# Performance work log

Hardware: AMD Instinct MI355X
Metric: run time of the kernel (lower is better)

Reference implementation:

```python
import math
import jax, jax.numpy as jnp
import numpy as np

K = 8
C = 16
MODES = 64
LEVELS = 0
CK = C * K


def _legendre_filters(k):
    """Numpy port of get_filter('legendre', k). Returns ec_s, ec_d, rc_e, rc_o (float32)."""
    from numpy.polynomial import Polynomial
    phi_c = np.zeros((k, k))
    phi2_c = np.zeros((k, k))
    for ki in range(k):
        P = np.polynomial.legendre.Legendre.basis(ki).convert(kind=Polynomial)
        c1 = P(Polynomial([-1.0, 2.0])).coef
        phi_c[ki, :len(c1)] = np.sqrt(2 * ki + 1) * c1
        c2 = P(Polynomial([-1.0, 4.0])).coef
        phi2_c[ki, :len(c2)] = np.sqrt(2.0) * np.sqrt(2 * ki + 1) * c2
    psi1 = phi2_c.copy()
    psi2 = phi2_c.copy()

    def proj_half(a, b):  # integral over [0,0.5] of poly product
        prod = np.convolve(a, b)
        prod[np.abs(prod) < 1e-10] = 0.0
        i = np.arange(len(prod))
        return np.sum(prod / (i + 1) * 0.5 ** (i + 1))

    for ki in range(k):
        a = phi2_c[ki, :ki + 1]
        for i in range(k):
            p = proj_half(a, phi_c[i, :i + 1])
            psi1[ki] -= p * phi_c[i]
            psi2[ki] -= p * phi_c[i]
        for j in range(ki):
            p = proj_half(a, psi1[j])
            psi1[ki] -= p * psi1[j]
            psi2[ki] -= p * psi2[j]
        prod1 = np.convolve(psi1[ki], psi1[ki])
        i1 = np.arange(len(prod1))
        norm1 = np.sum(prod1 / (i1 + 1) * 0.5 ** (i1 + 1))
        prod2 = np.convolve(psi2[ki], psi2[ki])
        i2 = np.arange(len(prod2))
        norm2 = np.sum(prod2 / (i2 + 1) * (1 - 0.5 ** (i2 + 1)))
        nrm = math.sqrt(max(norm1 + norm2, 1e-16))
        psi1[ki] /= nrm
        psi2[ki] /= nrm

    xg, wg = np.polynomial.legendre.leggauss(k)
    x_m = (xg + 1.0) / 2.0
    wm = wg / 2.0
    pv = lambda c, t: np.polynomial.polynomial.polyval(t, c)
    H0 = np.zeros((k, k)); H1 = np.zeros((k, k))
    G0 = np.zeros((k, k)); G1 = np.zeros((k, k))
    s2 = 1.0 / math.sqrt(2.0)
    for ki in range(k):
        for kp in range(k):
            pk = pv(phi_c[kp], x_m)
            H0[ki, kp] = s2 * np.sum(wm * pv(phi_c[ki], x_m / 2) * pk)
            G0[ki, kp] = s2 * np.sum(wm * pv(psi1[ki], x_m / 2) * pk)        # t<=0.5 -> psi1
            H1[ki, kp] = s2 * np.sum(wm * pv(phi_c[ki], (x_m + 1) / 2) * pk)
            G1[ki, kp] = s2 * np.sum(wm * pv(psi2[ki], (x_m + 1) / 2) * pk)  # t>0.5 -> psi2
    for m in (H0, H1, G0, G1):
        m[np.abs(m) < 1e-10] = 0.0
    # PHI0 = PHI1 = I, so H0r = H0 etc.
    ec_s = np.concatenate([H0.T, H1.T], axis=0).astype(np.float32)  # [2k,k]
    ec_d = np.concatenate([G0.T, G1.T], axis=0).astype(np.float32)
    rc_e = np.concatenate([H0, G0], axis=0).astype(np.float32)
    rc_o = np.concatenate([H1, G1], axis=0).astype(np.float32)
    return ec_s, ec_d, rc_e, rc_o


def setup_inputs() -> dict:
    key = jax.random.key(0)
    ks = jax.random.split(key, 7)
    B, N = 16, 8192
    x = jax.random.normal(ks[0], (B, N, C, K), dtype=jnp.float32)
    scale = 1.0 / (CK ** 0.5 + 1e-6)
    mk = lambda kk: scale * jax.random.normal(kk, (CK, CK, MODES), dtype=jnp.float32)
    ec_s, ec_d, rc_e, rc_o = _legendre_filters(K)
    return {
        "x": x,
        "A_wr": mk(ks[1]), "A_wi": mk(ks[2]),
        "B_wr": mk(ks[3]), "B_wi": mk(ks[4]),
        "C_wr": mk(ks[5]), "C_wi": mk(ks[6]),
        "ln_w": jnp.ones((CK,), jnp.float32),
        "ln_b": jnp.zeros((CK,), jnp.float32),
        "ec_s": jnp.asarray(ec_s), "ec_d": jnp.asarray(ec_d),
        "rc_e": jnp.asarray(rc_e), "rc_o": jnp.asarray(rc_o),
    }


def _spectral(v, wr, wi):
    # SparseKernelFT1d: rfft over N (ortho), truncate to `modes`, complex mix, irfft.
    b, n, c, k = v.shape
    vf = v.reshape(b, n, c * k)
    ft = jnp.fft.rfft(vf, axis=1, norm="ortho")           # [b, n//2+1, ck] complex
    l = min(MODES, ft.shape[1])
    w = wr[:, :, :l] + 1j * wi[:, :, :l]                   # [ck, ck, l]
    out = jnp.einsum("bxi,iox->bxo", ft[:, :l], w)
    out = jnp.pad(out, ((0, 0), (0, ft.shape[1] - l), (0, 0)))
    o = jnp.fft.irfft(out, n=n, axis=1, norm="ortho")
    return o.reshape(b, n, c, k)


def reference(x, A_wr, A_wi, B_wr, B_wi, C_wr, C_wi, ln_w, ln_b, ec_s, ec_d, rc_e, rc_o):
    B_, N0, c, k = x.shape
    nl = 2 ** math.ceil(math.log2(max(N0, 1)))
    if nl > N0:
        x = jnp.pad(x, ((0, 0), (0, nl - N0), (0, 0), (0, 0)))
    ns = int(math.log2(nl))
    Ud, Us = [], []
    for _ in range(ns - LEVELS):
        # one-level wavelet decomposition: even/odd gather + small [2k,k] matmuls
        xa = jnp.concatenate([x[:, ::2], x[:, 1::2]], axis=-1)  # [B, n/2, c, 2k]
        d = xa @ ec_d
        x = xa @ ec_s
        Ud.append(_spectral(d, A_wr, A_wi) + _spectral(x, B_wr, B_wi))
        Us.append(_spectral(d, C_wr, C_wi))
    # LayerNorm over flattened c*k, then exact GELU (torch default)
    b, n, cc, kk = x.shape
    xf = x.reshape(b, n, cc * kk)
    mu = jnp.mean(xf, axis=-1, keepdims=True)
    var = jnp.var(xf, axis=-1, keepdims=True)
    xf = (xf - mu) / jnp.sqrt(var + 1e-5) * ln_w + ln_b
    x = jax.nn.gelu(xf.reshape(b, n, cc, kk), approximate=False)
    for i in range(ns - 1 - LEVELS, -1, -1):
        x = x + Us[i]
        xc = jnp.concatenate([x, Ud[i]], axis=-1)              # [B, n, c, 2k]
        x_e = xc @ rc_e
        x_o = xc @ rc_o
        # interleave even/odd along N
        x = jnp.stack([x_e, x_o], axis=2).reshape(b, x_e.shape[1] * 2, cc, kk)
    return x[:, :N0]
```

## Files before the change

### kernel.cpp

```cpp
#include <hip/hip_runtime.h>
#include <math.h>

typedef unsigned short bfu;
typedef short bf16x8 __attribute__((ext_vector_type(8)));
typedef float f32x4 __attribute__((ext_vector_type(4)));

__device__ __forceinline__ float bs2f(bfu s){
  union{ unsigned int u; float f; } v; v.u = ((unsigned int)s) << 16; return v.f;
}
__device__ __forceinline__ bfu f2bs(float f){
  union{ float ff; unsigned int u; } v; v.ff = f;
  unsigned int u = v.u;
  unsigned int r = (u + 0x7fffu + ((u >> 16) & 1u)) >> 16;
  return (bfu)r;
}

struct LevelTab { int twoff[13]; int ll[13]; int logh[13]; };
struct WPtrs { const void* p[6]; };
struct FwTab { int pcum[7]; int h[6]; int np[6]; int twF[6]; long lvl[6]; long ftp[6]; };
struct DpTab { long lvl[7]; long ftp[7]; long yt[7]; int twD[7]; int h[7]; int l[7]; int lgh[7]; };
struct PrTab { int np[13]; int l[13]; long ftp[13]; long xa[13]; };
struct MxTab { int fcum[13]; int h[13]; long xa[13]; long yt[13]; };
struct IvTab { int bxcum[6]; int h[6]; int twF[6]; long yt[6]; long lvl[6]; };

__global__ __launch_bounds__(256) void k_sniff(const bfu* __restrict__ x, int* __restrict__ flag){
  __shared__ int cnt;
  if(threadIdx.x==0) cnt = 0;
  __syncthreads();
  int c = 0;
  for(int j=threadIdx.x; j<4096; j+=256){
    bfu v = x[2*j];
    int e = (v>>7)&0xFF;
    if(e >= 0xC0) c++;
  }
  atomicAdd(&cnt, c);
  __syncthreads();
  if(threadIdx.x==0) flag[0] = (cnt > 64) ? 1 : 0;
}

__global__ __launch_bounds__(256) void k_cvt_small(
    const void* lnw, const void* lnb, const void* ecs, const void* ecd,
    const void* rce, const void* rco, bfu* __restrict__ CSM, const int* __restrict__ FLAG){
  int f32 = FLAG[0];
  const void* src[6] = {ecs, ecd, rce, rco, lnw, lnb};
  int tid = threadIdx.x;
  for(int a=0; a<6; ++a)
    for(int j=tid; j<128; j+=256)
      CSM[a*128+j] = f32 ? f2bs(((const float*)src[a])[j]) : ((const bfu*)src[a])[j];
}

__global__ __launch_bounds__(256) void k_wtrans(WPtrs wp, bfu* __restrict__ W2, const int* __restrict__ FLAG){
  int f32 = FLAG[0];
  int o = blockIdx.x;
  int w = blockIdx.y;
  __shared__ bfu tile[64][130];
  int tid = threadIdx.x;
  const void* src = wp.p[w];
  if(f32){
    const float* s = (const float*)src;
    #pragma unroll
    for(int it=0; it<8; ++it){
      int e = it*256 + tid;
      int i = e >> 4, fq = e & 15;
      float4 v = *reinterpret_cast<const float4*>(s + ((size_t)i*128 + o)*64 + fq*4);
      tile[fq*4+0][i] = f2bs(v.x);
      tile[fq*4+1][i] = f2bs(v.y);
      tile[fq*4+2][i] = f2bs(v.z);
      tile[fq*4+3][i] = f2bs(v.w);
    }
  } else {
    const bfu* s = (const bfu*)src;
    #pragma unroll
    for(int it=0; it<4; ++it){
      int e = it*256 + tid;
      int i = e >> 3, fq = e & 7;
      union{uint4 u; bfu x[8];} U;
      U.u = *reinterpret_cast<const uint4*>(s + ((size_t)i*128 + o)*64 + fq*8);
      #pragma unroll
      for(int j=0;j<8;++j) tile[fq*8+j][i] = U.x[j];
    }
  }
  __syncthreads();
  bfu* dst = W2 + (size_t)w*64*128*128 + (size_t)o*128;
  #pragma unroll
  for(int it=0; it<8; ++it){
    int e = it*256 + tid;
    int f = e >> 5, iq = e & 31;
    union{uint2 u; bfu x[4];} P;
    #pragma unroll
    for(int j=0;j<4;++j) P.x[j] = tile[f][iq*4+j];
    *reinterpret_cast<uint2*>(dst + (size_t)f*128*128 + iq*4) = P.u;
  }
}

__global__ __launch_bounds__(256) void k_twgenF(bfu* __restrict__ TWF, bfu* __restrict__ TWI){
  int e = blockIdx.x*256 + threadIdx.x;
  int kind = blockIdx.y;
  const int offs[7] = {0,524288,786432,917504,983040,1015808,1032192};
  int le = 5;
  #pragma unroll
  for(int i=0;i<6;++i){ if(e < offs[i+1]){ le = i; break; } }
  int rem = e - offs[le];
  int logh = 12 - le;
  int h = 1 << logh;
  int f, t, neg;
  if(kind==0){ int r = rem >> logh; t = rem & (h-1); f = (r<64)?r:(r-64); neg = (r>=64); }
  else       { t = rem >> 7; int f2 = rem & 127;     f = (f2<64)?f2:(f2-64); neg = (f2>=64); }
  int m = (f*t) & (h-1);
  float th = 6.283185307179586f * ((float)m / (float)h);
  float s, c; sincosf(th, &s, &c);
  float val = neg ? -s : c;
  if(kind==0) TWF[e] = f2bs(val); else TWI[e] = f2bs(val);
}

__global__ __launch_bounds__(256) void k_twgen(LevelTab lt, float* __restrict__ tw){
  int lev = blockIdx.y;
  int logh = lt.logh[lev];
  int h = 1 << logh;
  int l = lt.ll[lev];
  int tot = l*h;
  int idx = blockIdx.x*256 + threadIdx.x;
  if(idx >= tot) return;
  int t = idx & (h-1);
  int f = idx >> logh;
  int m = (f*t) & (h-1);
  float th = 6.283185307179586f * ((float)m / (float)h);
  float s, c; sincosf(th, &s, &c);
  tw[lt.twoff[lev] + idx] = c;
  tw[lt.twoff[lev] + tot + idx] = s;
}

__global__ __launch_bounds__(256) void k_decomp0(
    const void* __restrict__ xin, bfu* __restrict__ dT, bfu* __restrict__ sT,
    const bfu* __restrict__ CSM, int h, const int* __restrict__ FLAG)
{
  int f32 = FLAG[0];
  __shared__ float ls[64][132];
  __shared__ bfu sdo[128][36];
  __shared__ bfu sso[128][36];
  __shared__ float Fd[16][8], Fs[16][8];
  int tid = threadIdx.x;
  if(tid < 128){ Fs[tid>>3][tid&7] = bs2f(CSM[tid]); Fd[tid>>3][tid&7] = bs2f(CSM[128+tid]); }
  int b = blockIdx.y;
  int t0in = blockIdx.x * 64;
  if(f32){
    const float* src = (const float*)xin + ((size_t)b*2*h + t0in)*128;
    #pragma unroll
    for(int it=0; it<8; ++it){
      int e = it*256 + tid;
      int row = e>>5, cq = e&31;
      float4 v = *reinterpret_cast<const float4*>(src + (size_t)row*128 + cq*4);
      ls[row][cq*4+0]=v.x; ls[row][cq*4+1]=v.y; ls[row][cq*4+2]=v.z; ls[row][cq*4+3]=v.w;
    }
  } else {
    const bfu* src = (const bfu*)xin + ((size_t)b*2*h + t0in)*128;
    #pragma unroll
    for(int it=0; it<4; ++it){
      int e = it*256 + tid;
      int row = e>>4, cq = e&15;
      union{uint4 u; bfu x[8];} U;
      U.u = *reinterpret_cast<const uint4*>(src + (size_t)row*128 + cq*8);
      #pragma unroll
      for(int j=0;j<8;++j) ls[row][cq*8+j] = bs2f(U.x[j]);
    }
  }
  __syncthreads();
  int g = tid>>7, ch = tid&127;
  int c = ch>>3, kp = ch&7;
  float fdE[8], fdO[8], fsE[8], fsO[8];
  #pragma unroll
  for(int j=0;j<8;++j){ fdE[j]=Fd[j][kp]; fdO[j]=Fd[8+j][kp]; fsE[j]=Fs[j][kp]; fsO[j]=Fs[8+j][kp]; }
  union{ uint2 u; bfu x[4]; } Dq, Sq;
  #pragma unroll
  for(int tl=0; tl<16; ++tl){
    int rl = 2*(g*16+tl);
    const float* ev = &ls[rl][c*8];
    const float* od = &ls[rl+1][c*8];
    float d=0.f, s=0.f;
    #pragma unroll
    for(int j=0;j<8;++j){
      d += ev[j]*fdE[j] + od[j]*fdO[j];
      s += ev[j]*fsE[j] + od[j]*fsO[j];
    }
    Dq.x[tl&3] = f2bs(d); Sq.x[tl&3] = f2bs(s);
    if((tl&3)==3){
      int tb = g*16 + (tl & ~3);
      *reinterpret_cast<uint2*>(&sdo[ch][tb]) = Dq.u;
      *reinterpret_cast<uint2*>(&sso[ch][tb]) = Sq.u;
    }
  }
  __syncthreads();
  size_t obase = (size_t)b*128*h + (t0in>>1);
  #pragma unroll
  for(int it=0; it<4; ++it){
    int e = it*256 + tid;
    int r = e >> 3, kq = e & 7;
    union{uint2 u; bfu x[4];} P;
    #pragma unroll
    for(int j=0;j<4;++j) P.x[j] = sdo[r][kq*4+j];
    *reinterpret_cast<uint2*>(dT + obase + (size_t)r*h + kq*4) = P.u;
  }
  #pragma unroll
  for(int it=0; it<4; ++it){
    int e = it*256 + tid;
    int r = e >> 3, kq = e & 7;
    union{uint2 u; bfu x[4];} P;
    #pragma unroll
    for(int j=0;j<4;++j) P.x[j] = sso[r][kq*4+j];
    *reinterpret_cast<uint2*>(sT + obase + (size_t)r*h + kq*4) = P.u;
  }
}

__global__ __launch_bounds__(256) void k_decompT_big(
    const bfu* __restrict__ inT, bfu* __restrict__ dT, bfu* __restrict__ sT,
    const bfu* __restrict__ CSM, int h)
{
  __shared__ float Fd[16][8], Fs[16][8];
  int tid = threadIdx.x;
  if(tid < 128){ Fs[tid>>3][tid&7] = bs2f(CSM[tid]); Fd[tid>>3][tid&7] = bs2f(CSM[128+tid]); }
  __syncthreads();
  int tt0 = blockIdx.x * 256;
  int b = blockIdx.y, c = blockIdx.z;
  int kp = tid >> 5, tq = tid & 31;
  float fdE[8], fdO[8], fsE[8], fsO[8];
  #pragma unroll
  for(int k=0;k<8;++k){ fdE[k]=Fd[k][kp]; fdO[k]=Fd[8+k][kp]; fsE[k]=Fs[k][kp]; fsO[k]=Fs[8+k][kp]; }
  const bfu* base = inT + ((size_t)b*128 + c*8)*(size_t)(2*h) + (size_t)2*tt0 + tq*16;
  union{uint4 u[2]; bfu x[16];} E[8];
  #pragma unroll
  for(int k=0;k<8;++k){
    E[k].u[0] = *reinterpret_cast<const uint4*>(base + (size_t)k*(2*h));
    E[k].u[1] = *reinterpret_cast<const uint4*>(base + (size_t)k*(2*h) + 8);
  }
  union{uint4 u; bfu x[8];} Od, Os;
  #pragma unroll
  for(int to=0; to<8; ++to){
    float d=0.f, s=0.f;
    #pragma unroll
    for(int k=0;k<8;++k){
      float ev = bs2f(E[k].x[2*to]), od = bs2f(E[k].x[2*to+1]);
      d += ev*fdE[k] + od*fdO[k];
      s += ev*fsE[k] + od*fsO[k];
    }
    Od.x[to] = f2bs(d); Os.x[to] = f2bs(s);
  }
  size_t ob = ((size_t)b*128 + c*8 + kp)*h + tt0 + tq*8;
  *reinterpret_cast<uint4*>(dT + ob) = Od.u;
  *reinterpret_cast<uint4*>(sT + ob) = Os.u;
}

__global__ __launch_bounds__(256) void k_decompT(
    const bfu* __restrict__ inT, bfu* __restrict__ dT, bfu* __restrict__ sT,
    const bfu* __restrict__ CSM, int h, int total)
{
  __shared__ float Fd[16][8], Fs[16][8];
  int tid = threadIdx.x;
  if(tid < 128){ Fs[tid>>3][tid&7] = bs2f(CSM[tid]); Fd[tid>>3][tid&7] = bs2f(CSM[128+tid]); }
  __syncthreads();
  int idx = blockIdx.x*256 + tid;
  if(idx >= total) return;
  if(h >= 4){
    int nto = h>>2;
    int to = idx & (nto-1);
    int bc = idx / nto;
    int c = bc & 15, b = bc >> 4;
    const bfu* base = inT + ((size_t)b*128 + c*8)*(size_t)(2*h) + to*8;
    float d8[4][8] = {}, s8[4][8] = {};
    #pragma unroll
    for(int k=0;k<8;++k){
      union{uint4 u; bfu x[8];} U;
      U.u = *reinterpret_cast<const uint4*>(base + (size_t)k*(2*h));
      const float* fdE = Fd[k]; const float* fdO = Fd[8+k];
      const float* fsE = Fs[k]; const float* fsO = Fs[8+k];
      #pragma unroll
      for(int tl=0; tl<4; ++tl){
        float ev = bs2f(U.x[2*tl]), od = bs2f(U.x[2*tl+1]);
        #pragma unroll
        for(int kp=0;kp<8;++kp){
          d8[tl][kp] += ev*fdE[kp] + od*fdO[kp];
          s8[tl][kp] += ev*fsE[kp] + od*fsO[kp];
        }
      }
    }
    #pragma unroll
    for(int kp=0;kp<8;++kp){
      union{uint2 u; bfu x[4];} Od, Os;
      #pragma unroll
      for(int tl=0;tl<4;++tl){ Od.x[tl]=f2bs(d8[tl][kp]); Os.x[tl]=f2bs(s8[tl][kp]); }
      size_t ob = ((size_t)b*128 + c*8 + kp)*h + to*4;
      *reinterpret_cast<uint2*>(dT + ob) = Od.u;
      *reinterpret_cast<uint2*>(sT + ob) = Os.u;
    }
  } else {
    int c = idx & 15, b = idx >> 4;
    const bfu* base = inT + ((size_t)b*128 + c*8)*(size_t)(2*h);
    for(int tl=0; tl<h; ++tl){
      float d8[8]={}, s8[8]={};
      for(int k=0;k<8;++k){
        float ev = bs2f(base[(size_t)k*2*h + 2*tl]);
        float od = bs2f(base[(size_t)k*2*h + 2*tl+1]);
        #pragma unroll
        for(int kp=0;kp<8;++kp){
          d8[kp] += ev*Fd[k][kp] + od*Fd[8+k][kp];
          s8[kp] += ev*Fs[k][kp] + od*Fs[8+k][kp];
        }
      }
      for(int kp=0;kp<8;++kp){
        size_t ob = ((size_t)b*128 + c*8 + kp)*h + tl;
        dT[ob] = f2bs(d8[kp]); sT[ob] = f2bs(s8[kp]);
      }
    }
  }
}

__global__ __launch_bounds__(256) void k_fwdft_all(
    const bfu* __restrict__ DTall, const bfu* __restrict__ STall,
    const bfu* __restrict__ TWF, float* __restrict__ FTPa, FwTab ft)
{
  int gp = blockIdx.x, b = blockIdx.y;
  int sig = blockIdx.z >> 1, rh = blockIdx.z & 1;
  int lev = 0;
  for(int i=5;i>0;--i){ if(gp >= ft.pcum[i]){ lev = i; break; } }
  int p = gp - ft.pcum[lev];
  int h = ft.h[lev];
  int Kpart = h / ft.np[lev];
  const bfu* SIG = (sig ? STall : DTall) + ft.lvl[lev] + (size_t)b*128*h;
  const bfu* TWr = TWF + ft.twF[lev] + (size_t)(rh*64)*h;
  __shared__ bfu lsA[64*72];
  __shared__ bfu lsB[128*72];
  int tid = threadIdx.x;
  int wave = tid>>6, lane = tid&63;
  int mh = (wave>>1)*32, nh = (wave&1)*64;
  int ml = lane&15, q = lane>>4;
  f32x4 acc[2][4];
  #pragma unroll
  for(int i=0;i<2;++i){
    #pragma unroll
    for(int j=0;j<4;++j) acc[i][j] = (f32x4)0.f;
  }
  int k0base = p*Kpart;
  for(int kc=0; kc<Kpart; kc+=64){
    int k0 = k0base + kc;
    #pragma unroll
    for(int it=0; it<2; ++it){
      int slot = it*256 + tid;
      int row = slot>>3, kq = slot&7;
      *reinterpret_cast<uint4*>(&lsA[row*72 + kq*8]) =
        *reinterpret_cast<const uint4*>(&TWr[(size_t)row*h + k0 + kq*8]);
    }
    #pragma unroll
    for(int it=0; it<4; ++it){
      int slot = it*256 + tid;
      int row = slot>>3, kq = slot&7;
      *reinterpret_cast<uint4*>(&lsB[row*72 + kq*8]) =
        *reinterpret_cast<const uint4*>(&SIG[(size_t)row*h + k0 + kq*8]);
    }
    __syncthreads();
    #pragma unroll
    for(int kk=0; kk<64; kk+=32){
      bf16x8 af[2], bfr[4];
      #pragma unroll
      for(int mi=0;mi<2;++mi)
        af[mi] = *reinterpret_cast<const bf16x8*>(&lsA[(mh+mi*16+ml)*72 + kk + q*8]);
      #pragma unroll
      for(int ni=0;ni<4;++ni)
        bfr[ni] = *reinterpret_cast<const bf16x8*>(&lsB[(nh+ni*16+ml)*72 + kk + q*8]);
      #pragma unroll
      for(int mi=0;mi<2;++mi){
        #pragma unroll
        for(int ni=0;ni<4;++ni)
          acc[mi][ni] = __builtin_amdgcn_mfma_f32_16x16x32_bf16(af[mi], bfr[ni], acc[mi][ni], 0,0,0);
      }
    }
    __syncthreads();
  }
  float* dst = FTPa + ft.ftp[lev] + (((size_t)p*2 + sig)*16 + b)*16384;
  #pragma unroll
  for(int mi=0;mi<2;++mi){
    #pragma unroll
    for(int ni=0;ni<4;++ni){
      int row = rh*64 + mh + mi*16 + q*4;
      int col = nh + ni*16 + ml;
      #pragma unroll
      for(int r=0;r<4;++r)
        dst[(size_t)(row+r)*128 + col] = acc[mi][ni][r];
    }
  }
}

__global__ __launch_bounds__(256) void k_fwdeep_all(
    const bfu* __restrict__ DTall, const bfu* __restrict__ STall,
    float* __restrict__ FTPa, const float* __restrict__ TWD, DpTab dp)
{
  int b = blockIdx.x, sig = blockIdx.y, j = blockIdx.z;
  int h = dp.h[j], l = dp.l[j], logh = dp.lgh[j];
  const bfu* src = (sig? STall : DTall) + dp.lvl[j] + (size_t)b*128*h;
  float* dst = FTPa + dp.ftp[j] + ((size_t)sig*16 + b)*16384;
  const float* TWc = TWD + dp.twD[j];
  __shared__ float s_sig[128*65];
  __shared__ float s_twc[33*64];
  __shared__ float s_tws[33*64];
  int tid = threadIdx.x;
  int hp = h + 1;
  for(int e = tid; e < 128*h; e += 256){
    int ch = e >> logh, t = e & (h-1);
    s_sig[ch*hp + t] = bs2f(src[e]);
  }
  int lh = l*h;
  const float* TWs = TWc + (size_t)lh;
  for(int e = tid; e < lh; e += 256){ s_twc[e] = TWc[e]; s_tws[e] = TWs[e]; }
  __syncthreads();
  for(int idx = tid; idx < l*128; idx += 256){
    int f = idx >> 7, ch = idx & 127;
    const float* sp = &s_sig[ch*hp];
    const float* cp = &s_twc[f*h];
    const float* zp = &s_tws[f*h];
    float re = 0.f, im = 0.f;
    for(int t=0; t<h; ++t){ float v = sp[t]; re += v*cp[t]; im -= v*zp[t]; }
    dst[(size_t)f*128 + ch] = re;
    dst[(size_t)(64+f)*128 + ch] = im;
  }
}

__global__ __launch_bounds__(256) void k_ftpred_all(
    const float* __restrict__ FTPa, bfu* __restrict__ XAa, PrTab pt)
{
  int lev = blockIdx.y;
  int e = blockIdx.x*256 + threadIdx.x;
  const size_t PS = (size_t)2*16*128*128;
  int ch4 = e & 31;
  int row = (e>>5) & 127;
  int b   = (e>>12) & 15;
  int sig = e>>16;
  int f = row & 63, im = row >> 6;
  if(f >= pt.l[lev]) return;
  const float* F = FTPa + pt.ftp[lev];
  int np = pt.np[lev];
  size_t src = (((size_t)sig*16 + b)*128 + row)*128 + (size_t)ch4*4;
  f32x4 v = *reinterpret_cast<const f32x4*>(&F[src]);
  for(int p=1;p<np;++p)
    v += *reinterpret_cast<const f32x4*>(&F[src + (size_t)p*PS]);
  int ch = ch4*4;
  union{ uint2 u; bfu x[4]; } P1, P3;
  #pragma unroll
  for(int j=0;j<4;++j){
    float vj = v[j];
    P1.x[j] = f2bs(im ? -vj : vj);
    P3.x[j] = f2bs(vj);
  }
  bfu* XA = XAa + pt.xa[lev];
  size_t base = (size_t)f*32*512;
  *reinterpret_cast<uint2*>(&XA[base + (size_t)b*512 + sig*256 + im*128 + ch]) = P1.u;
  *reinterpret_cast<uint2*>(&XA[base + (size_t)(16+b)*512 + sig*256 + (1-im)*128 + ch]) = P3.u;
}

__global__ __launch_bounds__(256) void k_modemix_all(
    const bfu* __restrict__ XAa, const bfu* __restrict__ W2,
    bfu* __restrict__ YTa, MxTab mt)
{
  int x = blockIdx.x;
  int lev = 0;
  for(int i=12;i>0;--i){ if(x >= mt.fcum[i]){ lev = i; break; } }
  int f = x - mt.fcum[lev];
  int h = mt.h[lev];
  int obase = blockIdx.y * 16;
  int tid = threadIdx.x;
  int wid = tid>>6, lane = tid&63;
  int m = wid & 1, part = wid >> 1;
  int ml = lane & 15, q = lane >> 4;
  const size_t WSZ = (size_t)64*128*128;
  const bfu* Ab = XAa + mt.xa[lev] + ((size_t)f*32 + m*16 + ml)*512 + q*8;
  const bfu* Wb = W2 + ((size_t)f*128 + obase + ml)*128 + q*8;
  f32x4 acc = (f32x4)0.f;
  if(part == 0){
    #pragma unroll
    for(int ks=0; ks<16; ++ks){
      bf16x8 A = *reinterpret_cast<const bf16x8*>(Ab + ks*32);
      bf16x8 B = *reinterpret_cast<const bf16x8*>(Wb + (size_t)(ks>>2)*WSZ + (ks&3)*32);
      acc = __builtin_amdgcn_mfma_f32_16x16x32_bf16(A, B, acc, 0,0,0);
    }
  } else {
    #pragma unroll
    for(int ks=0; ks<8; ++ks){
      bf16x8 A = *reinterpret_cast<const bf16x8*>(Ab + ks*32);
      bf16x8 B = *reinterpret_cast<const bf16x8*>(Wb + (size_t)(4 + (ks>>2))*WSZ + (ks&3)*32);
      acc = __builtin_amdgcn_mfma_f32_16x16x32_bf16(A, B, acc, 0,0,0);
    }
  }
  bool edge = (f==0) || (2*f == h);
  float sc = edge ? 1.0f/(float)h : 2.0f/(float)h;
  int fo = m ? (64+f) : f;
  int o = obase + ml;
  bfu* dst = YTa + mt.yt[lev] + (part ? (size_t)16*128*128 : 0);
  #pragma unroll
  for(int r=0;r<4;++r){
    int b = q*4 + r;
    float val = acc[r]*sc;
    if(m && edge) val = 0.f;
    dst[((size_t)b*128 + o)*128 + fo] = f2bs(val);
  }
}

__global__ __launch_bounds__(256) void k_invdft_all(
    const bfu* __restrict__ YTa, const bfu* __restrict__ TWI,
    bfu* __restrict__ UdAll, bfu* __restrict__ UsAll, IvTab iv)
{
  int x = blockIdx.x, b = blockIdx.y, u = blockIdx.z;
  int lev = 0;
  for(int i=5;i>0;--i){ if(x >= iv.bxcum[i]){ lev = i; break; } }
  int bx = x - iv.bxcum[lev];
  int h = iv.h[lev];
  bfu* outp = (u ? UsAll : UdAll) + iv.lvl[lev];
  const bfu* Y = YTa + iv.yt[lev] + ((size_t)u*16 + b)*16384;
  const bfu* TWIl = TWI + iv.twF[lev];
  int t0 = bx*128;
  __shared__ bfu lsA[128*136];
  __shared__ bfu lsB[128*136];
  int tid = threadIdx.x;
  #pragma unroll
  for(int it=0; it<8; ++it){
    int slot = it*256 + tid;
    int row = slot>>4, kq = slot&15;
    *reinterpret_cast<uint4*>(&lsA[row*136 + kq*8]) =
      *reinterpret_cast<const uint4*>(&TWIl[(size_t)(t0+row)*128 + kq*8]);
    *reinterpret_cast<uint4*>(&lsB[row*136 + kq*8]) =
      *reinterpret_cast<const uint4*>(&Y[(size_t)row*128 + kq*8]);
  }
  __syncthreads();
  int wave = tid>>6, lane = tid&63;
  int mh = (wave>>1)*64, nh = (wave&1)*64;
  int ml = lane&15, q = lane>>4;
  f32x4 acc[4][4];
  #pragma unroll
  for(int i=0;i<4;++i){
    #pragma unroll
    for(int j=0;j<4;++j) acc[i][j] = (f32x4)0.f;
  }
  #pragma unroll
  for(int kk=0; kk<128; kk+=32){
    bf16x8 af[4], bfr[4];
    #pragma unroll
    for(int mi=0;mi<4;++mi)
      af[mi] = *reinterpret_cast<const bf16x8*>(&lsA[(mh+mi*16+ml)*136 + kk + q*8]);
    #pragma unroll
    for(int ni=0;ni<4;++ni)
      bfr[ni] = *reinterpret_cast<const bf16x8*>(&lsB[(nh+ni*16+ml)*136 + kk + q*8]);
    #pragma unroll
    for(int mi=0;mi<4;++mi){
      #pragma unroll
      for(int ni=0;ni<4;++ni)
        acc[mi][ni] = __builtin_amdgcn_mfma_f32_16x16x32_bf16(af[mi], bfr[ni], acc[mi][ni], 0,0,0);
    }
  }
  #pragma unroll
  for(int mi=0;mi<4;++mi){
    #pragma unroll
    for(int ni=0;ni<4;++ni){
      int row = mh + mi*16 + q*4;
      int col = nh + ni*16 + ml;
      #pragma unroll
      for(int r=0;r<4;++r)
        outp[((size_t)b*h + t0+row+r)*128 + col] = f2bs(acc[mi][ni][r]);
    }
  }
}

__global__ __launch_bounds__(256) void k_invdeep_all(
    const bfu* __restrict__ YTa, bfu* __restrict__ UdAll, bfu* __restrict__ UsAll,
    const float* __restrict__ TWD, DpTab dp)
{
  int b = blockIdx.x, u = blockIdx.y, j = blockIdx.z;
  int h = dp.h[j], l = dp.l[j];
  bfu* outp = (u? UsAll : UdAll) + dp.lvl[j] + (size_t)b*h*128;
  const bfu* Y = YTa + dp.yt[j] + ((size_t)u*16 + b)*16384;
  const float* TWc = TWD + dp.twD[j];
  __shared__ float s_yr[128*66];
  __shared__ float s_yi[128*66];
  __shared__ float s_twc[33*64];
  __shared__ float s_tws[33*64];
  int tid = threadIdx.x;
  #pragma unroll
  for(int it=0; it<8; ++it){
    int slot = it*256 + tid;
    int ch = slot >> 4, kq = slot & 15;
    union{uint4 u4; bfu x[8];} U;
    U.u4 = *reinterpret_cast<const uint4*>(&Y[(size_t)ch*128 + kq*8]);
    if(kq < 8){
      #pragma unroll
      for(int jj=0;jj<8;++jj) s_yr[ch*66 + kq*8 + jj] = bs2f(U.x[jj]);
    } else {
      #pragma unroll
      for(int jj=0;jj<8;++jj) s_yi[ch*66 + (kq-8)*8 + jj] = bs2f(U.x[jj]);
    }
  }
  int lh = l*h;
  const float* TWs = TWc + (size_t)lh;
  for(int e = tid; e < lh; e += 256){ s_twc[e] = TWc[e]; s_tws[e] = TWs[e]; }
  __syncthreads();
  for(int idx = tid; idx < h*128; idx += 256){
    int t = idx >> 7, ch = idx & 127;
    const float* yr = &s_yr[ch*66];
    const float* yi = &s_yi[ch*66];
    float a = 0.f;
    for(int f=0; f<l; ++f)
      a += yr[f]*s_twc[f*h + t] - yi[f]*s_tws[f*h + t];
    outp[idx] = f2bs(a);
  }
}

__global__ __launch_bounds__(128) void k_lngelu(
    const bfu* __restrict__ xin, const bfu* __restrict__ CSM, bfu* __restrict__ xout)
{
  int b = blockIdx.x, tid = threadIdx.x;
  float v = bs2f(xin[b*128 + tid]);
  float s1 = v, s2 = v*v;
  #pragma unroll
  for(int o=32; o; o>>=1){ s1 += __shfl_down(s1,o); s2 += __shfl_down(s2,o); }
  __shared__ float red[2][2];
  int w = tid >> 6;
  if((tid & 63) == 0){ red[w][0]=s1; red[w][1]=s2; }
  __syncthreads();
  float m  = (red[0][0]+red[1][0]) * (1.0f/128.0f);
  float ms = (red[0][1]+red[1][1]) * (1.0f/128.0f);
  float var = ms - m*m;
  float xn = (v - m) * rsqrtf(var + 1e-5f) * bs2f(CSM[512+tid]) + bs2f(CSM[640+tid]);
  float g = 0.5f * xn * (1.0f + erff(xn * 0.70710678118654752f));
  xout[b*128 + tid] = f2bs(g);
}

__global__ __launch_bounds__(256) void k_recon(
    const bfu* __restrict__ xin, const bfu* __restrict__ usp, const bfu* __restrict__ udp,
    const bfu* __restrict__ CSM, void* __restrict__ xout, int h, int logh,
    int is_final, const int* __restrict__ FLAG)
{
  int f32 = is_final ? FLAG[0] : 0;
  __shared__ float Fe[16][8], Fo[16][8];
  int tid = threadIdx.x;
  if(tid < 128){ Fe[tid>>3][tid&7] = bs2f(CSM[256+tid]); Fo[tid>>3][tid&7] = bs2f(CSM[384+tid]); }
  __syncthreads();
  int idx = blockIdx.x*256 + tid;
  if(idx >= 16*h*16) return;
  int c  = idx & 15;
  int bt = idx >> 4;
  int t  = bt & (h-1);
  int b  = bt >> logh;
  size_t base = (((size_t)bt) << 7) + (c<<3);
  union{ uint4 u; bfu x[8]; } X, U, D;
  X.u = *reinterpret_cast<const uint4*>(xin + base);
  U.u = *reinterpret_cast<const uint4*>(usp + base);
  D.u = *reinterpret_cast<const uint4*>(udp + base);
  float y[16];
  #pragma unroll
  for(int j=0;j<8;++j){ y[j] = bs2f(X.x[j]) + bs2f(U.x[j]); y[8+j] = bs2f(D.x[j]); }
  float e8[8] = {0,0,0,0,0,0,0,0}, o8[8] = {0,0,0,0,0,0,0,0};
  #pragma unroll
  for(int j=0;j<16;++j){
    float v = y[j];
    #pragma unroll
    for(int k=0;k<8;++k){ e8[k] += v*Fe[j][k]; o8[k] += v*Fo[j][k]; }
  }
  size_t ob = (((size_t)(b*(h<<1) + (t<<1))) << 7) + (c<<3);
  if(f32){
    float* po = (float*)xout;
    *reinterpret_cast<float4*>(po + ob)       = make_float4(e8[0],e8[1],e8[2],e8[3]);
    *reinterpret_cast<float4*>(po + ob + 4)   = make_float4(e8[4],e8[5],e8[6],e8[7]);
    *reinterpret_cast<float4*>(po + ob + 128) = make_float4(o8[0],o8[1],o8[2],o8[3]);
    *reinterpret_cast<float4*>(po + ob + 132) = make_float4(o8[4],o8[5],o8[6],o8[7]);
  } else {
    union{ uint4 u; bfu x[8]; } Oe, Oo;
    #pragma unroll
    for(int k=0;k<8;++k){ Oe.x[k] = f2bs(e8[k]); Oo.x[k] = f2bs(o8[k]); }
    bfu* po = (bfu*)xout;
    *reinterpret_cast<uint4*>(po + ob)       = Oe.u;
    *reinterpret_cast<uint4*>(po + ob + 128) = Oo.u;
  }
}

extern "C" void kernel_launch(void* const* d_in, const int* in_sizes, int n_in,
                              void* d_out, int out_size, void* d_ws, size_t ws_size,
                              hipStream_t stream)
{
  (void)in_sizes; (void)n_in; (void)out_size; (void)ws_size;
  const void* x0 = d_in[0];
  WPtrs wp;
  for(int w=0;w<6;++w) wp.p[w] = d_in[1+w];

  char* ws = (char*)d_ws;
  size_t off = 0;
  auto carve = [&](size_t bytes)->char*{
    char* p = ws + off; off += (bytes + 255) & ~(size_t)255; return p; };

  int hv[13], lv[13], npv[13];
  const int offF[6] = {0,524288,786432,917504,983040,1015808};
  for(int i=0;i<13;++i){
    hv[i] = 4096 >> i;
    int l = hv[i]/2 + 1;
    lv[i] = (l < 64) ? l : 64;
    npv[i] = (i < 6) ? ((hv[i]/1024 > 0) ? hv[i]/1024 : 1) : 1;
  }
  long lvl[13]; long aTot = 0;
  for(int i=0;i<13;++i){ lvl[i] = aTot; aTot += (long)16*128*hv[i]; }
  long ftpo[13]; long fsl = 0;
  for(int i=0;i<13;++i){ ftpo[i] = fsl*524288L; fsl += npv[i]; }
  long xao[13]; long xsl = 0;
  for(int i=0;i<13;++i){ xao[i] = xsl; xsl += (long)lv[i]*16384; }
  long yto[13];
  for(int i=0;i<13;++i) yto[i] = (long)i*524288;

  int* FLAG = (int*)carve(256);
  bfu* CSM  = (bfu*)carve(2048);
  bfu* STall = (bfu*)carve((size_t)aTot*2);
  bfu* DTall = (bfu*)carve((size_t)aTot*2);
  bfu* UdAll = (bfu*)carve((size_t)aTot*2);
  bfu* UsAll = (bfu*)carve((size_t)aTot*2);
  bfu* WT   = (bfu*)carve((size_t)6*64*128*128*2);
  bfu* XAa  = (bfu*)carve((size_t)xsl*2);
  bfu* YTa  = (bfu*)carve((size_t)13*524288*2);
  bfu* TWF  = (bfu*)carve((size_t)1032192*2);
  bfu* TWI  = (bfu*)carve((size_t)1032192*2);
  float* FTPa = (float*)carve((size_t)fsl*524288*4);

  LevelTab lt;
  int acc = 0;
  for(int j=0;j<7;++j){
    int i = 6+j;
    lt.twoff[j]=acc; lt.ll[j]=lv[i]; lt.logh[j]=12-i;
    acc += 2*lv[i]*hv[i];
  }
  for(int j=7;j<13;++j){ lt.twoff[j]=0; lt.ll[j]=1; lt.logh[j]=0; }
  float* TWD = (float*)carve((size_t)acc*4);

  bfu* XPA = DTall;
  bfu* XPB = (bfu*)FTPa;

  FwTab ftb; { int pc=0;
    for(int i=0;i<6;++i){ ftb.pcum[i]=pc; pc+=npv[i]; ftb.h[i]=hv[i]; ftb.np[i]=npv[i];
                          ftb.twF[i]=offF[i]; ftb.lvl[i]=lvl[i]; ftb.ftp[i]=ftpo[i]; }
    ftb.pcum[6]=pc; }
  DpTab dpb;
  for(int j=0;j<7;++j){ int i=6+j;
    dpb.lvl[j]=lvl[i]; dpb.ftp[j]=ftpo[i]; dpb.yt[j]=yto[i]; dpb.twD[j]=lt.twoff[j];
    dpb.h[j]=hv[i]; dpb.l[j]=lv[i]; dpb.lgh[j]=12-i; }
  PrTab prb;
  for(int i=0;i<13;++i){ prb.np[i]=npv[i]; prb.l[i]=lv[i]; prb.ftp[i]=ftpo[i]; prb.xa[i]=xao[i]; }
  MxTab mxb; int fTot=0;
  for(int i=0;i<13;++i){ mxb.fcum[i]=fTot; fTot+=lv[i]; mxb.h[i]=hv[i]; mxb.xa[i]=xao[i]; mxb.yt[i]=yto[i]; }
  IvTab ivb; int bxTot=0;
  for(int i=0;i<6;++i){ ivb.bxcum[i]=bxTot; bxTot+=hv[i]/128; ivb.h[i]=hv[i];
                        ivb.twF[i]=offF[i]; ivb.yt[i]=yto[i]; ivb.lvl[i]=lvl[i]; }

  k_sniff<<<dim3(1),256,0,stream>>>((const bfu*)x0, FLAG);
  k_cvt_small<<<dim3(1),256,0,stream>>>(d_in[7], d_in[8], d_in[9], d_in[10], d_in[11], d_in[12], CSM, FLAG);
  k_wtrans<<<dim3(128,6),256,0,stream>>>(wp, WT, FLAG);
  k_twgenF<<<dim3(4032,2),256,0,stream>>>(TWF, TWI);
  k_twgen<<<dim3(17,7),256,0,stream>>>(lt, TWD);

  k_decomp0<<<dim3(hv[0]/32,16),256,0,stream>>>(x0, DTall+lvl[0], STall+lvl[0], CSM, hv[0], FLAG);
  for(int i=1;i<13;++i){
    int h = hv[i];
    const bfu* in = STall + lvl[i-1];
    bfu* dT = DTall + lvl[i];
    bfu* sT = STall + lvl[i];
    if(h >= 256){
      k_decompT_big<<<dim3(h/256,16,16),256,0,stream>>>(in, dT, sT, CSM, h);
    } else {
      int total = (h>=4) ? 16*16*(h>>2) : 256;
      k_decompT<<<dim3((total+255)/256),256,0,stream>>>(in, dT, sT, CSM, h, total);
    }
  }

  k_fwdft_all<<<dim3(ftb.pcum[6],16,4),256,0,stream>>>(DTall, STall, TWF, FTPa, ftb);
  k_fwdeep_all<<<dim3(16,2,7),256,0,stream>>>(DTall, STall, FTPa, TWD, dpb);

  k_ftpred_all<<<dim3(512,13),256,0,stream>>>(FTPa, XAa, prb);
  k_modemix_all<<<dim3(fTot,8),256,0,stream>>>(XAa, WT, YTa, mxb);

  k_invdft_all<<<dim3(bxTot,16,2),256,0,stream>>>(YTa, TWI, UdAll, UsAll, ivb);
  k_invdeep_all<<<dim3(16,2,7),256,0,stream>>>(YTa, UdAll, UsAll, TWD, dpb);

  k_lngelu<<<dim3(16),128,0,stream>>>(STall + lvl[12], CSM, XPA);
  bfu* rin = XPA;
  for(int i=12;i>=0;--i){
    int h = hv[i];
    void* rout = (i==0) ? d_out : (void*)((rin==XPA) ? XPB : XPA);
    int tot = 16*h*16;
    k_recon<<<dim3((tot+255)/256),256,0,stream>>>(rin, UsAll+lvl[i], UdAll+lvl[i], CSM, rout, h, 12-i, (i==0)?1:0, FLAG);
    rin = (bfu*)rout;
  }
}
```

Baseline: 514.7 us.

## Keep mode-mix weights in registers across levels and transpose output separately

The mode-mix kernel now launches one block per frequency and output tile, loads its weight fragments into registers once, and loops over all 13 levels. Each level's activations are staged through shared memory. Output is written with the output channel contiguous, so the scattered strided stores become coalesced, and a new transpose kernel restores the layout the inverse DFT expects. This cuts repeated weight reads across levels but adds an extra kernel launch, an extra buffer pass, and fewer blocks with a serial level loop.

```diff
diff --git a/kernel.cpp b/kernel.cpp
--- a/kernel.cpp
+++ b/kernel.cpp
@@ -20,7 +20,7 @@
 struct FwTab { int pcum[7]; int h[6]; int np[6]; int twF[6]; long lvl[6]; long ftp[6]; };
 struct DpTab { long lvl[7]; long ftp[7]; long yt[7]; int twD[7]; int h[7]; int l[7]; int lgh[7]; };
 struct PrTab { int np[13]; int l[13]; long ftp[13]; long xa[13]; };
-struct MxTab { int fcum[13]; int h[13]; long xa[13]; long yt[13]; };
+struct Mx2   { int lv[13]; int h[13]; long xa[13]; long yt[13]; };
 struct IvTab { int bxcum[6]; int h[6]; int twF[6]; long yt[6]; long lvl[6]; };
 
 __global__ __launch_bounds__(256) void k_sniff(const bfu* __restrict__ x, int* __restrict__ flag){
@@ -454,50 +454,97 @@
   *reinterpret_cast<uint2*>(&XA[base + (size_t)(16+b)*512 + sig*256 + (1-im)*128 + ch]) = P3.u;
 }
 
-__global__ __launch_bounds__(256) void k_modemix_all(
+__global__ __launch_bounds__(256) void k_modemix_lvl(
     const bfu* __restrict__ XAa, const bfu* __restrict__ W2,
-    bfu* __restrict__ YTa, MxTab mt)
-{
-  int x = blockIdx.x;
-  int lev = 0;
-  for(int i=12;i>0;--i){ if(x >= mt.fcum[i]){ lev = i; break; } }
-  int f = x - mt.fcum[lev];
-  int h = mt.h[lev];
+    bfu* __restrict__ YTp, Mx2 mt)
+{
+  int f = blockIdx.x;
   int obase = blockIdx.y * 16;
   int tid = threadIdx.x;
   int wid = tid>>6, lane = tid&63;
   int m = wid & 1, part = wid >> 1;
   int ml = lane & 15, q = lane >> 4;
   const size_t WSZ = (size_t)64*128*128;
-  const bfu* Ab = XAa + mt.xa[lev] + ((size_t)f*32 + m*16 + ml)*512 + q*8;
   const bfu* Wb = W2 + ((size_t)f*128 + obase + ml)*128 + q*8;
-  f32x4 acc = (f32x4)0.f;
+  bf16x8 wf[16];
   if(part == 0){
     #pragma unroll
-    for(int ks=0; ks<16; ++ks){
-      bf16x8 A = *reinterpret_cast<const bf16x8*>(Ab + ks*32);
-      bf16x8 B = *reinterpret_cast<const bf16x8*>(Wb + (size_t)(ks>>2)*WSZ + (ks&3)*32);
-      acc = __builtin_amdgcn_mfma_f32_16x16x32_bf16(A, B, acc, 0,0,0);
-    }
+    for(int ks=0; ks<16; ++ks)
+      wf[ks] = *reinterpret_cast<const bf16x8*>(Wb + (size_t)(ks>>2)*WSZ + (ks&3)*32);
   } else {
     #pragma unroll
-    for(int ks=0; ks<8; ++ks){
-      bf16x8 A = *reinterpret_cast<const bf16x8*>(Ab + ks*32);
-      bf16x8 B = *reinterpret_cast<const bf16x8*>(Wb + (size_t)(4 + (ks>>2))*WSZ + (ks&3)*32);
-      acc = __builtin_amdgcn_mfma_f32_16x16x32_bf16(A, B, acc, 0,0,0);
-    }
-  }
-  bool edge = (f==0) || (2*f == h);
-  float sc = edge ? 1.0f/(float)h : 2.0f/(float)h;
-  int fo = m ? (64+f) : f;
-  int o = obase + ml;
-  bfu* dst = YTa + mt.yt[lev] + (part ? (size_t)16*128*128 : 0);
-  #pragma unroll
-  for(int r=0;r<4;++r){
-    int b = q*4 + r;
-    float val = acc[r]*sc;
-    if(m && edge) val = 0.f;
-    dst[((size_t)b*128 + o)*128 + fo] = f2bs(val);
+    for(int ks=0; ks<8; ++ks)
+      wf[ks] = *reinterpret_cast<const bf16x8*>(Wb + (size_t)(4 + (ks>>2))*WSZ + (ks&3)*32);
+  }
+  __shared__ bfu lsA[32*520];
+  for(int lev=0; lev<13; ++lev){
+    if(f >= mt.lv[lev]) continue;
+    const bfu* Asrc = XAa + mt.xa[lev] + (size_t)f*16384;
+    #pragma unroll
+    for(int it=0; it<8; ++it){
+      int slot = it*256 + tid;
+      int row = slot>>6, kq = slot&63;
+      *reinterpret_cast<uint4*>(&lsA[row*520 + kq*8]) =
+        *reinterpret_cast<const uint4*>(&Asrc[(size_t)row*512 + kq*8]);
+    }
+    __syncthreads();
+    const bfu* Ar = &lsA[(m*16+ml)*520 + q*8];
+    f32x4 acc = (f32x4)0.f;
+    if(part == 0){
+      #pragma unroll
+      for(int ks=0; ks<16; ++ks){
+        bf16x8 A = *reinterpret_cast<const bf16x8*>(Ar + ks*32);
+        acc = __builtin_amdgcn_mfma_f32_16x16x32_bf16(A, wf[ks], acc, 0,0,0);
+      }
+    } else {
+      #pragma unroll
+      for(int ks=0; ks<8; ++ks){
+        bf16x8 A = *reinterpret_cast<const bf16x8*>(Ar + ks*32);
+        acc = __builtin_amdgcn_mfma_f32_16x16x32_bf16(A, wf[ks], acc, 0,0,0);
+      }
+    }
+    int h = mt.h[lev];
+    bool edge = (f==0) || (2*f == h);
+    float sc = edge ? 1.0f/(float)h : 2.0f/(float)h;
+    int fo = m ? (64+f) : f;
+    bfu* dst = YTp + mt.yt[lev] + (part ? (size_t)16*128*128 : 0);
+    #pragma unroll
+    for(int r=0;r<4;++r){
+      int b = q*4 + r;
+      float val = acc[r]*sc;
+      if(m && edge) val = 0.f;
+      dst[((size_t)b*128 + fo)*128 + obase + ml] = f2bs(val);
+    }
+    __syncthreads();
+  }
+}
+
+__global__ __launch_bounds__(256) void k_yttrans(
+    const bfu* __restrict__ YTp, bfu* __restrict__ YT2, Mx2 mt)
+{
+  int b = blockIdx.x, u = blockIdx.y, lev = blockIdx.z;
+  const bfu* src = YTp + mt.yt[lev] + ((size_t)u*16 + b)*16384;
+  bfu* dst = YT2 + mt.yt[lev] + ((size_t)u*16 + b)*16384;
+  __shared__ bfu tile[128][130];
+  int tid = threadIdx.x;
+  #pragma unroll
+  for(int it=0; it<8; ++it){
+    int slot = it*256 + tid;
+    int fo = slot>>4, kq = slot&15;
+    union{uint4 u4; bfu x[8];} U;
+    U.u4 = *reinterpret_cast<const uint4*>(&src[(size_t)fo*128 + kq*8]);
+    #pragma unroll
+    for(int j=0;j<8;++j) tile[kq*8+j][fo] = U.x[j];
+  }
+  __syncthreads();
+  #pragma unroll
+  for(int it=0; it<8; ++it){
+    int slot = it*256 + tid;
+    int ch = slot>>4, kq = slot&15;
+    union{uint4 u4; bfu x[8];} P;
+    #pragma unroll
+    for(int j=0;j<8;++j) P.x[j] = tile[ch][kq*8+j];
+    *reinterpret_cast<uint4*>(&dst[(size_t)ch*128 + kq*8]) = P.u4;
   }
 }
 
@@ -715,7 +762,8 @@
   bfu* UsAll = (bfu*)carve((size_t)aTot*2);
   bfu* WT   = (bfu*)carve((size_t)6*64*128*128*2);
   bfu* XAa  = (bfu*)carve((size_t)xsl*2);
-  bfu* YTa  = (bfu*)carve((size_t)13*524288*2);
+  bfu* YTp  = (bfu*)carve((size_t)13*524288*2);
+  bfu* YT2  = (bfu*)carve((size_t)13*524288*2);
   bfu* TWF  = (bfu*)carve((size_t)1032192*2);
   bfu* TWI  = (bfu*)carve((size_t)1032192*2);
   float* FTPa = (float*)carve((size_t)fsl*524288*4);
@@ -743,8 +791,8 @@
     dpb.h[j]=hv[i]; dpb.l[j]=lv[i]; dpb.lgh[j]=12-i; }
   PrTab prb;
   for(int i=0;i<13;++i){ prb.np[i]=npv[i]; prb.l[i]=lv[i]; prb.ftp[i]=ftpo[i]; prb.xa[i]=xao[i]; }
-  MxTab mxb; int fTot=0;
-  for(int i=0;i<13;++i){ mxb.fcum[i]=fTot; fTot+=lv[i]; mxb.h[i]=hv[i]; mxb.xa[i]=xao[i]; mxb.yt[i]=yto[i]; }
+  Mx2 mxb;
+  for(int i=0;i<13;++i){ mxb.lv[i]=lv[i]; mxb.h[i]=hv[i]; mxb.xa[i]=xao[i]; mxb.yt[i]=yto[i]; }
   IvTab ivb; int bxTot=0;
   for(int i=0;i<6;++i){ ivb.bxcum[i]=bxTot; bxTot+=hv[i]/128; ivb.h[i]=hv[i];
                         ivb.twF[i]=offF[i]; ivb.yt[i]=yto[i]; ivb.lvl[i]=lvl[i]; }
@@ -773,10 +821,11 @@
   k_fwdeep_all<<<dim3(16,2,7),256,0,stream>>>(DTall, STall, FTPa, TWD, dpb);
 
   k_ftpred_all<<<dim3(512,13),256,0,stream>>>(FTPa, XAa, prb);
-  k_modemix_all<<<dim3(fTot,8),256,0,stream>>>(XAa, WT, YTa, mxb);
-
-  k_invdft_all<<<dim3(bxTot,16,2),256,0,stream>>>(YTa, TWI, UdAll, UsAll, ivb);
-  k_invdeep_all<<<dim3(16,2,7),256,0,stream>>>(YTa, UdAll, UsAll, TWD, dpb);
+  k_modemix_lvl<<<dim3(64,8),256,0,stream>>>(XAa, WT, YTp, mxb);
+  k_yttrans<<<dim3(16,2,13),256,0,stream>>>(YTp, YT2, mxb);
+
+  k_invdft_all<<<dim3(bxTot,16,2),256,0,stream>>>(YT2, TWI, UdAll, UsAll, ivb);
+  k_invdeep_all<<<dim3(16,2,7),256,0,stream>>>(YT2, UdAll, UsAll, TWD, dpb);
 
   k_lngelu<<<dim3(16),128,0,stream>>>(STall + lvl[12], CSM, XPA);
   bfu* rin = XPA;
```

After: 503.2 us. -2.2%, faster.
